# Performance work log

Measured on AMD Instinct MI355X. Metric: run time of the kernel, lower is better.

Reference implementation:

```python
import jax, jax.numpy as jnp
import numpy as np

N_HEADS = 16


def setup_inputs() -> dict:
    key = jax.random.key(0)
    ks = jax.random.split(key, 12)
    B, S, D = 2, 2048, 1024
    inp = {
        "query": jax.random.normal(ks[0], (B, S, D), jnp.float32),
        "key": jax.random.normal(ks[1], (B, S, D), jnp.float32),
        "value": jax.random.normal(ks[2], (B, S, D), jnp.float32),
        "mask": jnp.ones((B, S), jnp.int32),
        "Wq": jax.random.normal(ks[3], (D, D), jnp.float32) * 0.02,
        "bq": jax.random.normal(ks[4], (D,), jnp.float32) * 0.02,
        "Wk": jax.random.normal(ks[5], (D, D), jnp.float32) * 0.02,
        "bk": jax.random.normal(ks[6], (D,), jnp.float32) * 0.02,
        "Wv": jax.random.normal(ks[7], (D, D), jnp.float32) * 0.02,
        "bv": jax.random.normal(ks[8], (D,), jnp.float32) * 0.02,
        "Wo": jax.random.normal(ks[9], (D, D), jnp.float32) * 0.02,
        "bo": jax.random.normal(ks[10], (D,), jnp.float32) * 0.02,
    }
    return inp


def _shape(x, bs, n_heads, d_head):
    # (bs, seq, dim) -> (bs, n_heads, seq, d_head)
    return x.reshape(bs, -1, n_heads, d_head).transpose(0, 2, 1, 3)


def reference(query, key, value, mask, Wq, bq, Wk, bk, Wv, bv, Wo, bo):
    bs, q_len, dim = query.shape
    d_head = dim // N_HEADS

    q = _shape(query @ Wq + bq, bs, N_HEADS, d_head) / jnp.sqrt(jnp.asarray(d_head, query.dtype))
    k = _shape(key @ Wk + bk, bs, N_HEADS, d_head)
    v = _shape(value @ Wv + bv, bs, N_HEADS, d_head)

    scores = jnp.einsum("bhqd,bhkd->bhqk", q, k)  # [bs, h, q_len, k_len]
    neg = jnp.finfo(scores.dtype).min
    scores = jnp.where((mask == 0)[:, None, None, :], neg, scores)
    weights = jax.nn.softmax(scores, axis=-1)  # dropout p=0 -> identity

    context = jnp.einsum("bhqk,bhkd->bhqd", weights, v)
    context = context.transpose(0, 2, 1, 3).reshape(bs, q_len, dim)
    return context @ Wo + bo
```

## Files before the change

kernel.cpp:

```cpp
#include <hip/hip_runtime.h>
#include <hip/hip_bf16.h>
#include <stdint.h>

typedef short s16x8 __attribute__((ext_vector_type(8)));
typedef float f32x4 __attribute__((ext_vector_type(4)));
typedef float f32x16 __attribute__((ext_vector_type(16)));

union FragU { uint4 u; s16x8 v; };

static __device__ __forceinline__ uint32_t pk2bf(float a, float b) {
  union { __hip_bfloat162 h; uint32_t u; } cv;
  cv.h = __float22bfloat162_rn(make_float2(a, b));
  return cv.u;
}

static __device__ __forceinline__ unsigned short f2bf(float f) {
  union { float f; uint32_t u; } x; x.f = f;
  uint32_t r = x.u + 0x7FFFu + ((x.u >> 16) & 1u);
  return (unsigned short)(r >> 16);
}

static __device__ __forceinline__ void gl_lds16(const void* g, void* lds_wave_base) {
  __builtin_amdgcn_global_load_lds(
      (const __attribute__((address_space(1))) uint32_t*)(uintptr_t)g,
      (__attribute__((address_space(3))) uint32_t*)(uintptr_t)lds_wave_base, 16, 0, 0);
}

__global__ __launch_bounds__(256) void wt4_kernel(const float* __restrict__ W0,
                                                  const float* __restrict__ W1,
                                                  const float* __restrict__ W2,
                                                  const float* __restrict__ W3,
                                                  unsigned short* __restrict__ T0,
                                                  unsigned short* __restrict__ T1,
                                                  unsigned short* __restrict__ T2,
                                                  unsigned short* __restrict__ T3) {
  __shared__ unsigned short tile[64][68];
  const int z = blockIdx.z;
  const float* W = (z == 0) ? W0 : (z == 1) ? W1 : (z == 2) ? W2 : W3;
  unsigned short* WT = (z == 0) ? T0 : (z == 1) ? T1 : (z == 2) ? T2 : T3;
  const int t = threadIdx.x;
  const int n0 = blockIdx.x * 64, k0 = blockIdx.y * 64;
  const int r = t >> 4, c4 = (t & 15) * 4;
#pragma unroll
  for (int i = 0; i < 4; ++i) {
    const int k = i * 16 + r;
    const float4 v = *(const float4*)&W[(k0 + k) * 1024 + n0 + c4];
    tile[k][c4 + 0] = f2bf(v.x);
    tile[k][c4 + 1] = f2bf(v.y);
    tile[k][c4 + 2] = f2bf(v.z);
    tile[k][c4 + 3] = f2bf(v.w);
  }
  __syncthreads();
#pragma unroll
  for (int i = 0; i < 4; ++i) {
    const int n = i * 16 + r;
    ushort4 o;
    o.x = tile[c4 + 0][n];
    o.y = tile[c4 + 1][n];
    o.z = tile[c4 + 2][n];
    o.w = tile[c4 + 3][n];
    *(ushort4*)&WT[(n0 + n) * 1024 + k0 + c4] = o;
  }
}

__global__ __launch_bounds__(256, 3) void qkv_gemm(const float* __restrict__ Aq,
                                                   const float* __restrict__ Ak,
                                                   const float* __restrict__ Av,
                                                   const unsigned short* __restrict__ Wq,
                                                   const unsigned short* __restrict__ Wk,
                                                   const unsigned short* __restrict__ Wv,
                                                   const float* __restrict__ bq,
                                                   const float* __restrict__ bk,
                                                   const float* __restrict__ bv,
                                                   unsigned short* __restrict__ Qb,
                                                   unsigned short* __restrict__ Kb,
                                                   unsigned short* __restrict__ Vt,
                                                   const float qscale) {
  __shared__ unsigned short As[2][128 * 32];
  __shared__ unsigned short Bs[2][128 * 32];
  const int t = threadIdx.x;
  const int z = blockIdx.z;
  const float* A = (z == 0) ? Aq : (z == 1) ? Ak : Av;
  const unsigned short* BT = (z == 0) ? Wq : (z == 1) ? Wk : Wv;
  const float* bias = (z == 0) ? bq : (z == 1) ? bk : bv;
  const float scale = (z == 0) ? qscale : 1.0f;

  const int lane = t & 63, w = t >> 6;
  const int g = lane >> 4, li = lane & 15;
  const int wr = (w >> 1) * 64, wc = (w & 1) * 64;
  const int lin = blockIdx.x + 8 * blockIdx.y;
  const int work = (lin & 7) * 32 + (lin >> 3);
  const int m0 = (work >> 3) * 128, n0 = (work & 7) * 128;

  const int arow = t >> 1, ac0 = (t & 1) * 2, asw = (arow >> 1) & 3;
  const int br1 = t >> 2, bg1 = (t & 3) ^ ((br1 >> 1) & 3);
  const int br2 = br1 + 64, bg2 = (t & 3) ^ ((br2 >> 1) & 3);

  auto stageB = [&](int k0, int buf) {
    gl_lds16(BT + (size_t)(n0 + br1) * 1024 + k0 + bg1 * 8, (char*)&Bs[buf][0] + (w << 10));
    gl_lds16(BT + (size_t)(n0 + br2) * 1024 + k0 + bg2 * 8, (char*)&Bs[buf][0] + 4096 + (w << 10));
  };

  uint4 ar0, ar1;
  auto loadA = [&](int k0) {
    const float* ga = A + (size_t)(m0 + arow) * 1024 + k0 + ac0 * 8;
    const float4 f0 = *(const float4*)(ga + 0), f1 = *(const float4*)(ga + 4);
    const float4 f2 = *(const float4*)(ga + 8), f3 = *(const float4*)(ga + 12);
    ar0 = uint4{pk2bf(f0.x, f0.y), pk2bf(f0.z, f0.w), pk2bf(f1.x, f1.y), pk2bf(f1.z, f1.w)};
    ar1 = uint4{pk2bf(f2.x, f2.y), pk2bf(f2.z, f2.w), pk2bf(f3.x, f3.y), pk2bf(f3.z, f3.w)};
  };
  auto storeA = [&](int buf) {
    char* ab = (char*)&As[buf][0] + arow * 64;
    *(uint4*)(ab + ((ac0 ^ asw) << 4)) = ar0;
    *(uint4*)(ab + (((ac0 + 1) ^ asw) << 4)) = ar1;
  };

  f32x4 acc[4][4] = {};
  stageB(0, 0);
  loadA(0);
  storeA(0);
  __syncthreads();
  int cur = 0;
  for (int k0 = 0; k0 < 1024; k0 += 32) {
    const bool more = (k0 + 32) < 1024;
    if (more) {
      stageB(k0 + 32, cur ^ 1);
      loadA(k0 + 32);
    }
    const char* Ab = (const char*)&As[cur][0];
    const char* Bb = (const char*)&Bs[cur][0];
    FragU a[4], bf[4];
#pragma unroll
    for (int i = 0; i < 4; ++i) {
      const int rowa = wr + i * 16 + li;
      a[i].u = *(const uint4*)(Ab + rowa * 64 + (((g) ^ ((rowa >> 1) & 3)) << 4));
      const int rowb = wc + i * 16 + li;
      bf[i].u = *(const uint4*)(Bb + rowb * 64 + (((g) ^ ((rowb >> 1) & 3)) << 4));
    }
#pragma unroll
    for (int fm = 0; fm < 4; ++fm)
#pragma unroll
      for (int fn = 0; fn < 4; ++fn)
        acc[fm][fn] = __builtin_amdgcn_mfma_f32_16x16x32_bf16(a[fm].v, bf[fn].v, acc[fm][fn], 0, 0, 0);
    if (more) storeA(cur ^ 1);
    __syncthreads();
    cur ^= 1;
  }

  unsigned short* OutN = (z == 0) ? Qb : Kb;
#pragma unroll
  for (int fn = 0; fn < 4; ++fn) {
    const int n = n0 + wc + fn * 16 + li;
    const float bv2 = bias[n];
#pragma unroll
    for (int fm = 0; fm < 4; ++fm) {
      const int mb = m0 + wr + fm * 16 + g * 4;
      const f32x4 v = acc[fm][fn];
      ushort4 pk;
      pk.x = f2bf((v[0] + bv2) * scale);
      pk.y = f2bf((v[1] + bv2) * scale);
      pk.z = f2bf((v[2] + bv2) * scale);
      pk.w = f2bf((v[3] + bv2) * scale);
      if (z == 2) {
        const int bb = mb >> 11, s = mb & 2047;
        *(ushort4*)&Vt[(size_t)(bb * 1024 + n) * 2048 + s] = pk;
      } else {
        unsigned short* o = OutN;
        o[(size_t)(mb + 0) * 1024 + n] = pk.x;
        o[(size_t)(mb + 1) * 1024 + n] = pk.y;
        o[(size_t)(mb + 2) * 1024 + n] = pk.z;
        o[(size_t)(mb + 3) * 1024 + n] = pk.w;
      }
    }
  }
}

__global__ __launch_bounds__(256, 3) void out_gemm(const unsigned short* __restrict__ A,
                                                   const unsigned short* __restrict__ BT,
                                                   const float* __restrict__ bias,
                                                   float* __restrict__ Out) {
  __shared__ unsigned short As[2][128 * 32];
  __shared__ unsigned short Bs[2][128 * 32];
  const int t = threadIdx.x;
  const int lane = t & 63, w = t >> 6;
  const int g = lane >> 4, li = lane & 15;
  const int wr = (w >> 1) * 64, wc = (w & 1) * 64;
  const int lin = blockIdx.x + 8 * blockIdx.y;
  const int work = (lin & 7) * 32 + (lin >> 3);
  const int m0 = (work >> 3) * 128, n0 = (work & 7) * 128;

  const int r1 = t >> 2, g1 = (t & 3) ^ ((r1 >> 1) & 3);
  const int r2 = r1 + 64, g2 = (t & 3) ^ ((r2 >> 1) & 3);

  auto stage = [&](int k0, int buf) {
    gl_lds16(BT + (size_t)(n0 + r1) * 1024 + k0 + g1 * 8, (char*)&Bs[buf][0] + (w << 10));
    gl_lds16(BT + (size_t)(n0 + r2) * 1024 + k0 + g2 * 8, (char*)&Bs[buf][0] + 4096 + (w << 10));
    gl_lds16(A + (size_t)(m0 + r1) * 1024 + k0 + g1 * 8, (char*)&As[buf][0] + (w << 10));
    gl_lds16(A + (size_t)(m0 + r2) * 1024 + k0 + g2 * 8, (char*)&As[buf][0] + 4096 + (w << 10));
  };

  f32x4 acc[4][4] = {};
  stage(0, 0);
  __syncthreads();
  int cur = 0;
  for (int k0 = 0; k0 < 1024; k0 += 32) {
    const bool more = (k0 + 32) < 1024;
    if (more) stage(k0 + 32, cur ^ 1);
    const char* Ab = (const char*)&As[cur][0];
    const char* Bb = (const char*)&Bs[cur][0];
    FragU a[4], bf[4];
#pragma unroll
    for (int i = 0; i < 4; ++i) {
      const int rowa = wr + i * 16 + li;
      a[i].u = *(const uint4*)(Ab + rowa * 64 + (((g) ^ ((rowa >> 1) & 3)) << 4));
      const int rowb = wc + i * 16 + li;
      bf[i].u = *(const uint4*)(Bb + rowb * 64 + (((g) ^ ((rowb >> 1) & 3)) << 4));
    }
#pragma unroll
    for (int fm = 0; fm < 4; ++fm)
#pragma unroll
      for (int fn = 0; fn < 4; ++fn)
        acc[fm][fn] = __builtin_amdgcn_mfma_f32_16x16x32_bf16(a[fm].v, bf[fn].v, acc[fm][fn], 0, 0, 0);
    __syncthreads();
    cur ^= 1;
  }

#pragma unroll
  for (int fn = 0; fn < 4; ++fn) {
    const int n = n0 + wc + fn * 16 + li;
    const float bv = bias[n];
#pragma unroll
    for (int fm = 0; fm < 4; ++fm) {
      const int mb = m0 + wr + fm * 16 + g * 4;
      const f32x4 v = acc[fm][fn];
#pragma unroll
      for (int r = 0; r < 4; ++r) Out[(size_t)(mb + r) * 1024 + n] = v[r] + bv;
    }
  }
}

__global__ __launch_bounds__(256, 2) void attn_kernel(const unsigned short* __restrict__ Qb,
                                                      const unsigned short* __restrict__ Kb,
                                                      const unsigned short* __restrict__ Vt,
                                                      const int* __restrict__ mask,
                                                      unsigned short* __restrict__ ctx) {
  __shared__ unsigned short Ks[2][64 * 64];
  __shared__ unsigned short Vs[2][64 * 64];
  const int t = threadIdx.x, lane = t & 63, w = t >> 6;
  const int l31 = lane & 31, hi = lane >> 5;
  const int d0 = blockIdx.x + 16 * blockIdx.y;
  const int work = (d0 & 7) * 64 + (d0 >> 3);
  const int qblk = work & 15, bh = work >> 4;
  const int b = bh >> 4, h = bh & 15;
  const int q0 = qblk * 128;
  const int qrow = b * 2048 + q0 + w * 32 + l31;

  const int srow = t >> 3, sch = t & 7;

  uint4 kr0, kr1, vr0, vr1;
  int mv = 1;
  auto loadKV = [&](int kvn) {
    const unsigned short* kbase = Kb + (size_t)(b * 2048 + kvn) * 1024 + h * 64;
    kr0 = *(const uint4*)(kbase + (size_t)srow * 1024 + sch * 8);
    kr1 = *(const uint4*)(kbase + (size_t)(srow + 32) * 1024 + sch * 8);
    const unsigned short* vbase = Vt + (size_t)(b * 1024 + h * 64) * 2048 + kvn;
    vr0 = *(const uint4*)(vbase + (size_t)srow * 2048 + sch * 8);
    vr1 = *(const uint4*)(vbase + (size_t)(srow + 32) * 2048 + sch * 8);
    mv = mask[b * 2048 + kvn + lane];
  };
  auto storeKV = [&](int buf) {
    char* kb = (char*)&Ks[buf][0];
    char* vb = (char*)&Vs[buf][0];
    const int o0 = srow * 128 + ((sch * 16) ^ ((srow & 7) << 4));
    const int o1 = (srow + 32) * 128 + ((sch * 16) ^ ((srow & 7) << 4));
    *(uint4*)(kb + o0) = kr0;
    *(uint4*)(kb + o1) = kr1;
    *(uint4*)(vb + o0) = vr0;
    *(uint4*)(vb + o1) = vr1;
  };

  FragU qf[4];
  {
    const unsigned short* qb = Qb + (size_t)qrow * 1024 + h * 64 + hi * 8;
#pragma unroll
    for (int dc = 0; dc < 4; ++dc) qf[dc].u = *(const uint4*)(qb + dc * 16);
  }

  loadKV(0);
  storeKV(0);
  __syncthreads();

  f32x16 acc[2] = {};
  float m_run = 8.0f, l_run = 0.f;
  int cur = 0;

  for (int tile = 0; tile < 32; ++tile) {
    const bool more = tile + 1 < 32;
    const int mvcur = mv;
    if (more) loadKV((tile + 1) * 64);

    f32x16 sc[2] = {};
    {
      const char* kb = (const char*)&Ks[cur][0];
      __builtin_amdgcn_s_setprio(1);
#pragma unroll
      for (int t2 = 0; t2 < 2; ++t2) {
        const int row = t2 * 32 + l31;
        const int sw = (row & 7) << 4;
        const int rb = row * 128;
#pragma unroll
        for (int dc = 0; dc < 4; ++dc) {
          FragU kf;
          kf.u = *(const uint4*)(kb + rb + ((16 * (dc * 2 + hi)) ^ sw));
          sc[t2] = __builtin_amdgcn_mfma_f32_32x32x16_bf16(kf.v, qf[dc].v, sc[t2], 0, 0, 0);
        }
      }
      __builtin_amdgcn_s_setprio(0);
    }

    if (!__all(mvcur != 0)) {
#pragma unroll
      for (int t2 = 0; t2 < 2; ++t2)
#pragma unroll
        for (int r = 0; r < 16; ++r) {
          const int kvv = t2 * 32 + (r & 3) + 8 * (r >> 2) + 4 * hi;
          sc[t2][r] += (__shfl(mvcur, kvv, 64) ? 0.f : -30000.f);
        }
    }

    float pm = sc[0][0];
#pragma unroll
    for (int t2 = 0; t2 < 2; ++t2)
#pragma unroll
      for (int r = 0; r < 16; ++r) pm = fmaxf(pm, sc[t2][r]);
    pm = fmaxf(pm, __shfl_xor(pm, 32, 64));

    if (!__all(pm <= m_run + 8.f)) {
      const float m_new = fmaxf(m_run, pm);
      const float rsc = __builtin_amdgcn_exp2f(m_run - m_new);
      m_run = m_new;
      l_run *= rsc;
#pragma unroll
      for (int dt = 0; dt < 2; ++dt)
#pragma unroll
        for (int r = 0; r < 16; ++r) acc[dt][r] *= rsc;
    }

    float rs = 0.f;
#pragma unroll
    for (int t2 = 0; t2 < 2; ++t2)
#pragma unroll
      for (int r = 0; r < 16; ++r) {
        const float e = __builtin_amdgcn_exp2f(sc[t2][r] - m_run);
        sc[t2][r] = e;
        rs += e;
      }
    l_run += rs;

    FragU pf[4];
#pragma unroll
    for (int ks = 0; ks < 4; ++ks) {
      const int t2 = ks >> 1, s8 = (ks & 1) * 8;
      uint32_t U = pk2bf(sc[t2][s8 + 0], sc[t2][s8 + 1]);
      uint32_t V2 = pk2bf(sc[t2][s8 + 2], sc[t2][s8 + 3]);
      uint32_t X = pk2bf(sc[t2][s8 + 4], sc[t2][s8 + 5]);
      uint32_t Y = pk2bf(sc[t2][s8 + 6], sc[t2][s8 + 7]);
      asm("v_permlane32_swap_b32 %0, %1" : "+v"(U), "+v"(X));
      asm("v_permlane32_swap_b32 %0, %1" : "+v"(V2), "+v"(Y));
      pf[ks].u = uint4{U, V2, X, Y};
    }

    {
      const char* vb = (const char*)&Vs[cur][0];
      __builtin_amdgcn_s_setprio(1);
#pragma unroll
      for (int dt = 0; dt < 2; ++dt) {
        const int drow = dt * 32 + l31;
        const int sw = (drow & 7) << 4;
        const int rb = drow * 128;
#pragma unroll
        for (int ks = 0; ks < 4; ++ks) {
          FragU vf;
          vf.u = *(const uint4*)(vb + rb + ((16 * (ks * 2 + hi)) ^ sw));
          acc[dt] = __builtin_amdgcn_mfma_f32_32x32x16_bf16(vf.v, pf[ks].v, acc[dt], 0, 0, 0);
        }
      }
      __builtin_amdgcn_s_setprio(0);
    }

    if (more) storeKV(cur ^ 1);
    __syncthreads();
    cur ^= 1;
  }

  const float l_tot = l_run + __shfl_xor(l_run, 32, 64);
  const float inv_l = 1.0f / l_tot;
  unsigned short* cb = ctx + (size_t)qrow * 1024 + h * 64;
#pragma unroll
  for (int dt = 0; dt < 2; ++dt)
#pragma unroll
    for (int rq = 0; rq < 4; ++rq) {
      uint2 o;
      o.x = pk2bf(acc[dt][rq * 4 + 0] * inv_l, acc[dt][rq * 4 + 1] * inv_l);
      o.y = pk2bf(acc[dt][rq * 4 + 2] * inv_l, acc[dt][rq * 4 + 3] * inv_l);
      *(uint2*)(cb + dt * 32 + rq * 8 + hi * 4) = o;
    }
}

extern "C" void kernel_launch(void* const* d_in, const int* in_sizes, int n_in,
                              void* d_out, int out_size, void* d_ws, size_t ws_size,
                              hipStream_t stream) {
  const float* query = (const float*)d_in[0];
  const float* key = (const float*)d_in[1];
  const float* value = (const float*)d_in[2];
  const int* mask = (const int*)d_in[3];
  const float* Wq = (const float*)d_in[4];
  const float* bq = (const float*)d_in[5];
  const float* Wk = (const float*)d_in[6];
  const float* bk = (const float*)d_in[7];
  const float* Wv = (const float*)d_in[8];
  const float* bv = (const float*)d_in[9];
  const float* Wo = (const float*)d_in[10];
  const float* bo = (const float*)d_in[11];
  float* out = (float*)d_out;

  const size_t MB = 1024 * 1024;
  if (ws_size < 40 * MB) return;
  char* ws = (char*)d_ws;
  unsigned short* WqT = (unsigned short*)(ws);
  unsigned short* WkT = (unsigned short*)(ws + 2 * MB);
  unsigned short* WvT = (unsigned short*)(ws + 4 * MB);
  unsigned short* WoT = (unsigned short*)(ws + 6 * MB);
  unsigned short* Qb = (unsigned short*)(ws + 8 * MB);
  unsigned short* Kb = (unsigned short*)(ws + 16 * MB);
  unsigned short* Vt = (unsigned short*)(ws + 24 * MB);
  unsigned short* ctx = (unsigned short*)(ws + 32 * MB);

  const dim3 tb(256);
  wt4_kernel<<<dim3(16, 16, 4), tb, 0, stream>>>(Wq, Wk, Wv, Wo, WqT, WkT, WvT, WoT);

  const float qscale = 0.125f * 1.4426950408889634f;
  qkv_gemm<<<dim3(8, 32, 3), tb, 0, stream>>>(query, key, value, WqT, WkT, WvT,
                                              bq, bk, bv, Qb, Kb, Vt, qscale);

  attn_kernel<<<dim3(16, 32), tb, 0, stream>>>(Qb, Kb, Vt, mask, ctx);

  out_gemm<<<dim3(8, 32), tb, 0, stream>>>(ctx, WoT, bo, out);
}
```

Measured before the change: 118.7 us.

## Triple-buffer GEMM pipelines and stage fp32 A via direct global-to-LDS loads

Both projection GEMMs move from double to triple buffering. They prefetch two k-tiles ahead and use explicit vmcnt waits plus a raw s_barrier in place of __syncthreads. In qkv_gemm the fp32 activations are now copied straight into LDS with global_load_lds through a swizzled layout, then converted to bf16 when fragments are read from LDS. This replaces the register round trip of load, convert and store. The cost is more LDS per block (occupancy hint drops from 3 to 2), repeated conversion work per wave, and more fragile manual wait counts.

After: 139.2 us. 17.2% more time.

```diff
diff --git a/kernel.cpp b/kernel.cpp
--- a/kernel.cpp
+++ b/kernel.cpp
@@ -63,7 +63,7 @@
   }
 }
 
-__global__ __launch_bounds__(256, 3) void qkv_gemm(const float* __restrict__ Aq,
+__global__ __launch_bounds__(256, 2) void qkv_gemm(const float* __restrict__ Aq,
                                                    const float* __restrict__ Ak,
                                                    const float* __restrict__ Av,
                                                    const unsigned short* __restrict__ Wq,
@@ -76,8 +76,8 @@
                                                    unsigned short* __restrict__ Kb,
                                                    unsigned short* __restrict__ Vt,
                                                    const float qscale) {
-  __shared__ unsigned short As[2][128 * 32];
-  __shared__ unsigned short Bs[2][128 * 32];
+  __shared__ char AsB[3][128 * 128];
+  __shared__ char BsB[3][128 * 64];
   const int t = threadIdx.x;
   const int z = blockIdx.z;
   const float* A = (z == 0) ? Aq : (z == 1) ? Ak : Av;
@@ -92,59 +92,68 @@
   const int work = (lin & 7) * 32 + (lin >> 3);
   const int m0 = (work >> 3) * 128, n0 = (work & 7) * 128;
 
-  const int arow = t >> 1, ac0 = (t & 1) * 2, asw = (arow >> 1) & 3;
   const int br1 = t >> 2, bg1 = (t & 3) ^ ((br1 >> 1) & 3);
   const int br2 = br1 + 64, bg2 = (t & 3) ^ ((br2 >> 1) & 3);
-
-  auto stageB = [&](int k0, int buf) {
-    gl_lds16(BT + (size_t)(n0 + br1) * 1024 + k0 + bg1 * 8, (char*)&Bs[buf][0] + (w << 10));
-    gl_lds16(BT + (size_t)(n0 + br2) * 1024 + k0 + bg2 * 8, (char*)&Bs[buf][0] + 4096 + (w << 10));
+  int arow[4], acol[4];
+#pragma unroll
+  for (int i = 0; i < 4; ++i) {
+    const int c = t + 256 * i;
+    const int row = c >> 3, sl = (c >> 1) & 3, hf = c & 1;
+    arow[i] = row;
+    acol[i] = ((sl ^ (row & 3)) << 3) + ((hf ^ ((row >> 2) & 1)) << 2);
+  }
+
+  auto stage = [&](int kt, int buf) {
+    const int k0 = kt * 32;
+    char* bb = &BsB[buf][0] + (w << 10);
+    gl_lds16(BT + (size_t)(n0 + br1) * 1024 + k0 + bg1 * 8, bb);
+    gl_lds16(BT + (size_t)(n0 + br2) * 1024 + k0 + bg2 * 8, bb + 4096);
+#pragma unroll
+    for (int i = 0; i < 4; ++i)
+      gl_lds16(A + (size_t)(m0 + arow[i]) * 1024 + k0 + acol[i],
+               &AsB[buf][0] + i * 4096 + (w << 10));
   };
 
-  uint4 ar0, ar1;
-  auto loadA = [&](int k0) {
-    const float* ga = A + (size_t)(m0 + arow) * 1024 + k0 + ac0 * 8;
-    const float4 f0 = *(const float4*)(ga + 0), f1 = *(const float4*)(ga + 4);
-    const float4 f2 = *(const float4*)(ga + 8), f3 = *(const float4*)(ga + 12);
-    ar0 = uint4{pk2bf(f0.x, f0.y), pk2bf(f0.z, f0.w), pk2bf(f1.x, f1.y), pk2bf(f1.z, f1.w)};
-    ar1 = uint4{pk2bf(f2.x, f2.y), pk2bf(f2.z, f2.w), pk2bf(f3.x, f3.y), pk2bf(f3.z, f3.w)};
-  };
-  auto storeA = [&](int buf) {
-    char* ab = (char*)&As[buf][0] + arow * 64;
-    *(uint4*)(ab + ((ac0 ^ asw) << 4)) = ar0;
-    *(uint4*)(ab + (((ac0 + 1) ^ asw) << 4)) = ar1;
-  };
-
   f32x4 acc[4][4] = {};
-  stageB(0, 0);
-  loadA(0);
-  storeA(0);
-  __syncthreads();
+  stage(0, 0);
+  stage(1, 1);
+  asm volatile("s_waitcnt vmcnt(6)" ::: "memory");
+  asm volatile("s_barrier" ::: "memory");
+
   int cur = 0;
-  for (int k0 = 0; k0 < 1024; k0 += 32) {
-    const bool more = (k0 + 32) < 1024;
-    if (more) {
-      stageB(k0 + 32, cur ^ 1);
-      loadA(k0 + 32);
-    }
-    const char* Ab = (const char*)&As[cur][0];
-    const char* Bb = (const char*)&Bs[cur][0];
+  for (int kt = 0; kt < 32; ++kt) {
+    if (kt < 30) {
+      int nb = cur + 2; if (nb >= 3) nb -= 3;
+      stage(kt + 2, nb);
+    }
+    const char* Ab = &AsB[cur][0];
+    const char* Bb = &BsB[cur][0];
     FragU a[4], bf[4];
 #pragma unroll
     for (int i = 0; i < 4; ++i) {
-      const int rowa = wr + i * 16 + li;
-      a[i].u = *(const uint4*)(Ab + rowa * 64 + (((g) ^ ((rowa >> 1) & 3)) << 4));
-      const int rowb = wc + i * 16 + li;
-      bf[i].u = *(const uint4*)(Bb + rowb * 64 + (((g) ^ ((rowb >> 1) & 3)) << 4));
+      const int ra = wr + i * 16 + li;
+      const int hsw = ((ra >> 2) & 1) << 4;
+      const char* pa = Ab + ra * 128 + ((g ^ (ra & 3)) << 5);
+      const float4 fa0 = *(const float4*)(pa + hsw);
+      const float4 fa1 = *(const float4*)(pa + (16 ^ hsw));
+      a[i].u = uint4{pk2bf(fa0.x, fa0.y), pk2bf(fa0.z, fa0.w),
+                     pk2bf(fa1.x, fa1.y), pk2bf(fa1.z, fa1.w)};
+      const int rb = wc + i * 16 + li;
+      bf[i].u = *(const uint4*)(Bb + rb * 64 + ((g ^ ((rb >> 1) & 3)) << 4));
     }
 #pragma unroll
     for (int fm = 0; fm < 4; ++fm)
 #pragma unroll
       for (int fn = 0; fn < 4; ++fn)
         acc[fm][fn] = __builtin_amdgcn_mfma_f32_16x16x32_bf16(a[fm].v, bf[fn].v, acc[fm][fn], 0, 0, 0);
-    if (more) storeA(cur ^ 1);
-    __syncthreads();
-    cur ^= 1;
+
+    if (kt < 30) {
+      asm volatile("s_waitcnt vmcnt(6)" ::: "memory");
+    } else if (kt == 30) {
+      asm volatile("s_waitcnt vmcnt(0)" ::: "memory");
+    }
+    if (kt < 31) asm volatile("s_barrier" ::: "memory");
+    cur = (cur == 2) ? 0 : cur + 1;
   }
 
   unsigned short* OutN = (z == 0) ? Qb : Kb;
@@ -175,12 +184,12 @@
   }
 }
 
-__global__ __launch_bounds__(256, 3) void out_gemm(const unsigned short* __restrict__ A,
+__global__ __launch_bounds__(256, 2) void out_gemm(const unsigned short* __restrict__ A,
                                                    const unsigned short* __restrict__ BT,
                                                    const float* __restrict__ bias,
                                                    float* __restrict__ Out) {
-  __shared__ unsigned short As[2][128 * 32];
-  __shared__ unsigned short Bs[2][128 * 32];
+  __shared__ char AsB[3][128 * 64];
+  __shared__ char BsB[3][128 * 64];
   const int t = threadIdx.x;
   const int lane = t & 63, w = t >> 6;
   const int g = lane >> 4, li = lane & 15;
@@ -192,37 +201,49 @@
   const int r1 = t >> 2, g1 = (t & 3) ^ ((r1 >> 1) & 3);
   const int r2 = r1 + 64, g2 = (t & 3) ^ ((r2 >> 1) & 3);
 
-  auto stage = [&](int k0, int buf) {
-    gl_lds16(BT + (size_t)(n0 + r1) * 1024 + k0 + g1 * 8, (char*)&Bs[buf][0] + (w << 10));
-    gl_lds16(BT + (size_t)(n0 + r2) * 1024 + k0 + g2 * 8, (char*)&Bs[buf][0] + 4096 + (w << 10));
-    gl_lds16(A + (size_t)(m0 + r1) * 1024 + k0 + g1 * 8, (char*)&As[buf][0] + (w << 10));
-    gl_lds16(A + (size_t)(m0 + r2) * 1024 + k0 + g2 * 8, (char*)&As[buf][0] + 4096 + (w << 10));
+  auto stage = [&](int kt, int buf) {
+    const int k0 = kt * 32;
+    gl_lds16(BT + (size_t)(n0 + r1) * 1024 + k0 + g1 * 8, &BsB[buf][0] + (w << 10));
+    gl_lds16(BT + (size_t)(n0 + r2) * 1024 + k0 + g2 * 8, &BsB[buf][0] + 4096 + (w << 10));
+    gl_lds16(A + (size_t)(m0 + r1) * 1024 + k0 + g1 * 8, &AsB[buf][0] + (w << 10));
+    gl_lds16(A + (size_t)(m0 + r2) * 1024 + k0 + g2 * 8, &AsB[buf][0] + 4096 + (w << 10));
   };
 
   f32x4 acc[4][4] = {};
   stage(0, 0);
-  __syncthreads();
+  stage(1, 1);
+  asm volatile("s_waitcnt vmcnt(4)" ::: "memory");
+  asm volatile("s_barrier" ::: "memory");
+
   int cur = 0;
-  for (int k0 = 0; k0 < 1024; k0 += 32) {
-    const bool more = (k0 + 32) < 1024;
-    if (more) stage(k0 + 32, cur ^ 1);
-    const char* Ab = (const char*)&As[cur][0];
-    const char* Bb = (const char*)&Bs[cur][0];
+  for (int kt = 0; kt < 32; ++kt) {
+    if (kt < 30) {
+      int nb = cur + 2; if (nb >= 3) nb -= 3;
+      stage(kt + 2, nb);
+    }
+    const char* Ab = &AsB[cur][0];
+    const char* Bb = &BsB[cur][0];
     FragU a[4], bf[4];
 #pragma unroll
     for (int i = 0; i < 4; ++i) {
-      const int rowa = wr + i * 16 + li;
-      a[i].u = *(const uint4*)(Ab + rowa * 64 + (((g) ^ ((rowa >> 1) & 3)) << 4));
-      const int rowb = wc + i * 16 + li;
-      bf[i].u = *(const uint4*)(Bb + rowb * 64 + (((g) ^ ((rowb >> 1) & 3)) << 4));
+      const int ra = wr + i * 16 + li;
+      a[i].u = *(const uint4*)(Ab + ra * 64 + ((g ^ ((ra >> 1) & 3)) << 4));
+      const int rb = wc + i * 16 + li;
+      bf[i].u = *(const uint4*)(Bb + rb * 64 + ((g ^ ((rb >> 1) & 3)) << 4));
     }
 #pragma unroll
     for (int fm = 0; fm < 4; ++fm)
 #pragma unroll
       for (int fn = 0; fn < 4; ++fn)
         acc[fm][fn] = __builtin_amdgcn_mfma_f32_16x16x32_bf16(a[fm].v, bf[fn].v, acc[fm][fn], 0, 0, 0);
-    __syncthreads();
-    cur ^= 1;
+
+    if (kt < 30) {
+      asm volatile("s_waitcnt vmcnt(4)" ::: "memory");
+    } else if (kt == 30) {
+      asm volatile("s_waitcnt vmcnt(0)" ::: "memory");
+    }
+    if (kt < 31) asm volatile("s_barrier" ::: "memory");
+    cur = (cur == 2) ? 0 : cur + 1;
   }
 
 #pragma unroll
```
